# Optimization experiments

Hardware: AMD Instinct MI355X
Metric: run time of the kernel (lower is better)

Reference implementation:

```python
import jax, jax.numpy as jnp
import numpy as np

B = 32            # batch size
N = 100           # n_nodes (== MAX_N_NODES here)
MAXN = 100        # MAX_N_NODES
H = 256           # HIDDEN_DIM_FEATURES_EXTRACTOR
HA = 1024         # HIDDEN_DIM_ACTOR
HC = 512          # HIDDEN_DIM_CRITIC
K_ACTIVE = 5000   # exact number of active mask entries per batch element


def setup_inputs() -> dict:
    key = jax.random.key(0)
    ks = jax.random.split(key, 16)
    feat = jax.random.normal(ks[0], (B, N + 1, H), jnp.float32)
    # mask: exactly K_ACTIVE ones among N*N per batch row (dim == K for all rows)
    rng = np.random.default_rng(0)
    mask = np.zeros((B, N * N), np.float32)
    for i in range(B):
        mask[i, rng.choice(N * N, size=K_ACTIVE, replace=False)] = 1.0
    mask = jnp.asarray(mask).reshape(B, N, N)
    ext_mask = jnp.concatenate([jnp.zeros((B, 1, N), jnp.float32), mask], axis=1)  # [B, N+1, N]
    embedded_features = jnp.concatenate([feat, ext_mask], axis=2)  # [B, N+1, H+N]

    def lin(k, fi, fo):
        s = 1.0 / np.sqrt(fi)
        return (jax.random.uniform(k, (fi, fo), jnp.float32, -s, s),
                jax.random.uniform(jax.random.fold_in(k, 1), (fo,), jnp.float32, -s, s))

    aW1, ab1 = lin(ks[1], 3 * H, HA)
    aW2, ab2 = lin(ks[2], HA, HA)
    aW3, ab3 = lin(ks[3], HA, 1)
    cW1, cb1 = lin(ks[4], H, HC)
    cW2, cb2 = lin(ks[5], HC, HC)
    cW3, cb3 = lin(ks[6], HC, 1)
    return dict(embedded_features=embedded_features,
                aW1=aW1, ab1=ab1, aW2=aW2, ab2=ab2, aW3=aW3, ab3=ab3,
                cW1=cW1, cb1=cb1, cW2=cW2, cb2=cb2, cW3=cW3, cb3=cb3,
                K=K_ACTIVE)


def reference(embedded_features, aW1, ab1, aW2, ab2, aW3, ab3,
              cW1, cb1, cW2, cb2, cW3, cb3, K):
    # decompose features
    gn = embedded_features[:, :, :H]
    ext_mask = embedded_features[:, :, H:]
    g = gn[:, :1, :]                      # [B,1,H] graph embedding
    nodes = gn[:, 1:, :]                  # [B,N,H] node embeddings
    mask = ext_mask[:, 1:, :].reshape(B, -1)  # [B, N*N]

    # indexes of active pairs (stable top_k -> ascending indices among ones, like nonzero)
    _, idx = jax.lax.top_k(mask, K)       # [B,K] int32
    idx1 = idx // N
    idx2 = idx % N
    n1 = jnp.take_along_axis(nodes, idx1[:, :, None], axis=1)  # [B,K,H]
    n2 = jnp.take_along_axis(nodes, idx2[:, :, None], axis=1)  # [B,K,H]
    pairs = jnp.concatenate([jnp.broadcast_to(g, (B, K, H)), n1, n2], axis=-1)  # [B,K,3H]

    # actor MLP (tanh hidden activations)
    h = jnp.tanh(pairs @ aW1 + ab1)
    h = jnp.tanh(h @ aW2 + ab2)
    logits = h @ aW3 + ab3                # [B,K,1]
    pi = jax.nn.softmax(logits, axis=1)   # softmax over the K gathered pairs

    # scatter back into padded grid
    shaped = jnp.zeros((B, N * N), pi.dtype).at[jnp.arange(B)[:, None], idx].set(pi[..., 0])
    filled = jnp.zeros((B, MAXN, MAXN), pi.dtype).at[:, :N, :N].set(shaped.reshape(B, N, N))
    filled = filled.reshape(B, MAXN * MAXN)

    # critic MLP on graph embedding
    hv = jnp.tanh(g @ cW1 + cb1)
    hv = jnp.tanh(hv @ cW2 + cb2)
    value = hv @ cW3 + cb3                # [B,1,1]
    return filled, value
```

## Files before the change

### kernel.cpp

```cpp
#include <hip/hip_runtime.h>
#include <stdint.h>

#define AS1 __attribute__((address_space(1)))
#define AS3 __attribute__((address_space(3)))

typedef __bf16 bf16x8 __attribute__((ext_vector_type(8)));
typedef float  f32x4  __attribute__((ext_vector_type(4)));
typedef int    i32x4  __attribute__((ext_vector_type(4)));
typedef int    i32x8  __attribute__((ext_vector_type(8)));
typedef float  f32x16 __attribute__((ext_vector_type(16)));

__device__ __forceinline__ float tanh_fast(float x){
    float e = __expf(2.0f * x);
    return 1.0f - 2.0f * __builtin_amdgcn_rcpf(e + 1.0f);
}
__device__ __forceinline__ float tanh4_fast(float x){
    float e = __expf(2.0f * x);
    return fmaf(-8.0f, __builtin_amdgcn_rcpf(e + 1.0f), 4.0f);
}

__device__ __forceinline__ unsigned short f2bf(float f){
    unsigned int u = __float_as_uint(f);
    u = (u + 0x7fffu + ((u >> 16) & 1u)) >> 16;
    return (unsigned short)u;
}

template<int SEL>
__device__ __forceinline__ unsigned int pk4(unsigned int old, float a, float b){
#if defined(__has_builtin) && __has_builtin(__builtin_amdgcn_cvt_scalef32_pk_fp4_f32)
    return __builtin_amdgcn_cvt_scalef32_pk_fp4_f32(old, a, b, 1.0f, SEL);
#else
    float fa = fabsf(a), fb = fabsf(b);
    unsigned int ma = fa < 0.25f ? 0u : fa < 0.75f ? 1u : fa < 1.25f ? 2u :
                      fa < 1.75f ? 3u : fa < 2.5f  ? 4u : fa < 3.5f  ? 5u :
                      fa < 5.0f  ? 6u : 7u;
    unsigned int mb = fb < 0.25f ? 0u : fb < 0.75f ? 1u : fb < 1.25f ? 2u :
                      fb < 1.75f ? 3u : fb < 2.5f  ? 4u : fb < 3.5f  ? 5u :
                      fb < 5.0f  ? 6u : 7u;
    ma |= (a < 0.0f ? 8u : 0u); mb |= (b < 0.0f ? 8u : 0u);
    return old | ((ma | (mb << 4)) << (8 * SEL));
#endif
}

__device__ __forceinline__ i32x8 lo4(i32x4 a){
    return __builtin_shufflevector(a, a, 0, 1, 2, 3, -1, -1, -1, -1);
}

#define B2F(u, lo, hi) { lo = __uint_as_float((u) << 16); hi = __uint_as_float((u) & 0xffff0000u); }

__global__ __launch_bounds__(256) void k_stage1(
    const float* __restrict__ ef,  const float* __restrict__ aW1, const float* __restrict__ ab1,
    const float* __restrict__ aW2,
    const float* __restrict__ cW1, const float* __restrict__ cb1,
    const float* __restrict__ cW2, const float* __restrict__ cb2,
    const float* __restrict__ cW3, const float* __restrict__ cb3,
    int* __restrict__ pairs, unsigned char* __restrict__ w2b,
    unsigned short* __restrict__ P, float* __restrict__ out, int* __restrict__ qctr)
{
    int blk = blockIdx.x;
    int t = threadIdx.x;
    __shared__ __align__(16) unsigned short an[112 * 264];
    __shared__ float gsh[256], gpart[4][64];
    __shared__ int s_base, s_woff[4], s_wc[4];
    __shared__ float gs[256], h1[512], h2[512], wred[4];

    if (blk == 1024 && t == 0) qctr[0] = 0;

    if (blk < 1024){
        int cb = blk & 15, s = (blk >> 4) & 1, b = blk >> 5;
        for (int e = t; e < 25600; e += 256){
            int row = e >> 8, col = e & 255;
            an[row * 264 + col] = f2bf(ef[(size_t)b * 35956 + (size_t)(1 + row) * 356 + col]);
        }
        for (int e = t; e < 3168; e += 256) an[26400 + e] = 0;
        gsh[t] = ef[(size_t)b * 35956 + t];
        __syncthreads();

        if (s == 0){
            int cl = t & 63, q = t >> 6;
            const float* a1p = aW1 + (size_t)(q * 64) * 1024 + cb * 64 + cl;
            float p = 0.f;
            for (int i = 0; i < 64; ++i) p += gsh[q * 64 + i] * a1p[(size_t)i * 1024];
            gpart[q][cl] = p;
        }
        __syncthreads();

        int w = t >> 6, lane = t & 63, quad = lane >> 4, n = lane & 15;
        int c = cb * 64 + w * 16 + n;
        bf16x8 bfr[8];
        const float* wp = aW1 + (size_t)(256 + s * 256 + quad * 8) * 1024 + c;
#pragma unroll
        for (int kt = 0; kt < 8; ++kt){
            unsigned int ww[4];
#pragma unroll
            for (int jj = 0; jj < 4; ++jj){
                unsigned short lo = f2bf(wp[(size_t)(kt * 32 + 2 * jj) * 1024]);
                unsigned short hi = f2bf(wp[(size_t)(kt * 32 + 2 * jj + 1) * 1024]);
                ww[jj] = (unsigned int)lo | ((unsigned int)hi << 16);
            }
            uint4 pk = make_uint4(ww[0], ww[1], ww[2], ww[3]);
            bfr[kt] = *(bf16x8*)&pk;
        }
        f32x4 acc[7];
#pragma unroll
        for (int m = 0; m < 7; ++m){ f32x4 z = {0.f, 0.f, 0.f, 0.f}; acc[m] = z; }
#pragma unroll
        for (int kt = 0; kt < 8; ++kt){
#pragma unroll
            for (int m = 0; m < 7; ++m){
                const bf16x8* ap = (const bf16x8*)(an + (m * 16 + n) * 264 + kt * 32 + quad * 8);
                acc[m] = __builtin_amdgcn_mfma_f32_16x16x32_bf16(*ap, bfr[kt], acc[m], 0, 0, 0);
            }
        }
        int cw = w * 16 + n;
        float addv = (s == 0)
            ? (gpart[0][cw] + gpart[1][cw] + gpart[2][cw] + gpart[3][cw] + ab1[c]) : 0.0f;
        size_t base = (size_t)s * 3276800 + (size_t)b * 102400;
#pragma unroll
        for (int m = 0; m < 7; ++m){
            int r0 = m * 16 + quad * 4;
#pragma unroll
            for (int r = 0; r < 4; ++r){
                int row = r0 + r;
                if (row < 100) P[base + (size_t)row * 1024 + c] = f2bf(acc[m][r] + addv);
            }
        }
    } else if (blk < 1056){
        int b = blk - 1024;
        if (t == 0) s_base = 0;
        __syncthreads();
        int lane = t & 63, w = t >> 6;
        for (int ch = 0; ch < 40; ++ch){
            int pos = ch * 256 + t;
            bool valid = false;
            if (pos < 10000){
                int r = pos / 100, c = pos - (pos / 100) * 100;
                valid = ef[(size_t)b * 35956 + (size_t)(1 + r) * 356 + 256 + c] != 0.0f;
            }
            unsigned long long bal = __ballot(valid);
            if (lane == 0) s_wc[w] = __popcll(bal);
            __syncthreads();
            if (t == 0){
                int r = s_base;
                for (int q = 0; q < 4; ++q){ s_woff[q] = r; r += s_wc[q]; }
                s_base = r;
            }
            __syncthreads();
            if (valid){
                int rank = __popcll(bal & ((1ull << lane) - 1ull));
                int o = s_woff[w] + rank;
                if (o < 5000) pairs[b * 5000 + o] = pos;
            }
            __syncthreads();
        }
    } else if (blk < 1184){
        int tid = (blk - 1056) * 256 + t;
        int lane = tid & 63, kt = (tid >> 6) & 15, ct = tid >> 10;
        int lh = lane >> 5, n = lane & 31;
        const float* src = aW2 + (size_t)(kt * 64 + lh * 32) * 1024 + ct * 32 + n;
        unsigned int d[4] = {0u, 0u, 0u, 0u};
#pragma unroll
        for (int j = 0; j < 32; ++j){
            float a = src[(size_t)j * 1024] * 128.0f;
            float f = fabsf(a);
            unsigned int m = f < 0.25f ? 0u : f < 0.75f ? 1u : f < 1.25f ? 2u :
                             f < 1.75f ? 3u : f < 2.5f  ? 4u : f < 3.5f  ? 5u :
                             f < 5.0f  ? 6u : 7u;
            unsigned int nib = m | (a < 0.0f ? 8u : 0u);
            d[j >> 3] |= nib << (4 * (j & 7));
        }
        *(uint4*)(w2b + (size_t)(ct * 16 + kt) * 1024 + lane * 16) =
            make_uint4(d[0], d[1], d[2], d[3]);
    } else {
        int b = blk - 1184;
        gs[t] = ef[(size_t)b * 35956 + t];
        __syncthreads();
        for (int o = t; o < 512; o += 256){
            float a = cb1[o];
            for (int i = 0; i < 256; ++i) a += gs[i] * cW1[(size_t)i * 512 + o];
            h1[o] = tanh_fast(a);
        }
        __syncthreads();
        for (int o = t; o < 512; o += 256){
            float a = cb2[o];
            for (int i = 0; i < 512; ++i) a += h1[i] * cW2[(size_t)i * 512 + o];
            h2[o] = tanh_fast(a);
        }
        __syncthreads();
        float p = h2[t] * cW3[t] + h2[t + 256] * cW3[t + 256];
        for (int m = 32; m >= 1; m >>= 1) p += __shfl_xor(p, m);
        if ((t & 63) == 0) wred[t >> 6] = p;
        __syncthreads();
        if (t == 0) out[320000 + b] = wred[0] + wred[1] + wred[2] + wred[3] + cb3[0];
    }
}

__global__ __launch_bounds__(256, 4) void k_main(
    const int* __restrict__ pairs,
    const unsigned short* __restrict__ P1, const unsigned short* __restrict__ P2,
    const unsigned char* __restrict__ w2b, const float* __restrict__ ab2,
    const float* __restrict__ aW3, float* __restrict__ logits, int* __restrict__ qctr)
{
    __shared__ __align__(16) unsigned char wbuf[2][16384];
    __shared__ int s_tile;
    int t = threadIdx.x, w = t >> 6, lane = t & 63;
    int lrow = lane & 31, lh = lane >> 5;
    int soff = w * 4096 + lane * 16;

    for (;;){
        if (t == 0) s_tile = atomicAdd(qctr, 1);
        __syncthreads();
        int tt = s_tile;
        if (tt >= 1280) break;
        int b = tt / 40, tile = tt - b * 40;

        {
            const unsigned char* s = w2b + soff;
            unsigned char* d = &wbuf[0][0] + soff;
#pragma unroll
            for (int i = 0; i < 4; ++i)
                __builtin_amdgcn_global_load_lds((AS1 void*)(s + i * 1024),
                                                 (AS3 void*)(d + i * 1024), 16, 0, 0);
        }

        int grow = tile * 128 + w * 32 + lrow;
        int pidx = pairs[b * 5000 + (grow < 5000 ? grow : 4999)];
        int i1 = pidx / 100, i2 = pidx - i1 * 100;
        const uint4* pa = (const uint4*)(P1 + (((size_t)(b * 100 + i1)) << 10)) + lh * 4;
        const uint4* pb = (const uint4*)(P2 + (((size_t)(b * 100 + i2)) << 10)) + lh * 4;

        i32x4 af4[16];
#pragma unroll
        for (int kt = 0; kt < 16; ++kt){
            uint4 qa[4], qb[4];
#pragma unroll
            for (int j = 0; j < 4; ++j){ qa[j] = pa[kt * 8 + j]; qb[j] = pb[kt * 8 + j]; }
            unsigned int d[4];
#pragma unroll
            for (int j = 0; j < 4; ++j){
                float a0, a1, b0, b1;
                unsigned int dd = 0;
                B2F(qa[j].x, a0, a1); B2F(qb[j].x, b0, b1);
                dd = pk4<0>(dd, tanh4_fast(a0 + b0), tanh4_fast(a1 + b1));
                B2F(qa[j].y, a0, a1); B2F(qb[j].y, b0, b1);
                dd = pk4<1>(dd, tanh4_fast(a0 + b0), tanh4_fast(a1 + b1));
                B2F(qa[j].z, a0, a1); B2F(qb[j].z, b0, b1);
                dd = pk4<2>(dd, tanh4_fast(a0 + b0), tanh4_fast(a1 + b1));
                B2F(qa[j].w, a0, a1); B2F(qb[j].w, b0, b1);
                dd = pk4<3>(dd, tanh4_fast(a0 + b0), tanh4_fast(a1 + b1));
                d[j] = dd;
            }
            i32x4 f = {(int)d[0], (int)d[1], (int)d[2], (int)d[3]};
            af4[kt] = f;
        }

        float prt[16];
#pragma unroll
        for (int r = 0; r < 16; ++r) prt[r] = 0.f;
        f32x16 acc0, acc1;

        for (int ct = 0; ct < 32; ++ct){
            __syncthreads();
            if (ct < 31){
                const unsigned char* sp = w2b + (size_t)(ct + 1) * 16384 + soff;
                unsigned char* d = &wbuf[(ct + 1) & 1][0] + soff;
#pragma unroll
                for (int i = 0; i < 4; ++i)
                    __builtin_amdgcn_global_load_lds((AS1 void*)(sp + i * 1024),
                                                     (AS3 void*)(d + i * 1024), 16, 0, 0);
            }
#pragma unroll
            for (int r = 0; r < 16; ++r){ acc0[r] = 0.f; acc1[r] = 0.f; }
            const unsigned char* bb = &wbuf[ct & 1][0] + lane * 16;
#pragma unroll
            for (int j = 0; j < 8; ++j){
                uint4 q0 = *(const uint4*)(bb + (2 * j) * 1024);
                uint4 q1 = *(const uint4*)(bb + (2 * j + 1) * 1024);
                i32x4 b0 = {(int)q0.x, (int)q0.y, (int)q0.z, (int)q0.w};
                i32x4 b1 = {(int)q1.x, (int)q1.y, (int)q1.z, (int)q1.w};
                acc0 = __builtin_amdgcn_mfma_scale_f32_32x32x64_f8f6f4(
                           lo4(af4[2 * j]),     lo4(b0), acc0, 4, 4, 0, 0x7D7D7D7D, 0, 0x78787878);
                acc1 = __builtin_amdgcn_mfma_scale_f32_32x32x64_f8f6f4(
                           lo4(af4[2 * j + 1]), lo4(b1), acc1, 4, 4, 0, 0x7D7D7D7D, 0, 0x78787878);
            }
            int c = ct * 32 + lrow;
            float w3 = aW3[c], bias = ab2[c];
#pragma unroll
            for (int r = 0; r < 16; ++r)
                prt[r] += tanh_fast(acc0[r] + acc1[r] + bias) * w3;
        }

#pragma unroll
        for (int r = 0; r < 16; ++r){
            float v = prt[r];
            v += __shfl_xor(v, 1); v += __shfl_xor(v, 2); v += __shfl_xor(v, 4);
            v += __shfl_xor(v, 8); v += __shfl_xor(v, 16);
            if (lrow == 0){
                int row = (r & 3) + 8 * (r >> 2) + 4 * lh;
                int g = tile * 128 + w * 32 + row;
                if (g < 5000) logits[b * 5000 + g] = v;
            }
        }
    }
}

__global__ void k_soft(const float* __restrict__ logits, const int* __restrict__ pairs,
                       float* __restrict__ out){
    int b = blockIdx.x, t = threadIdx.x;
    __shared__ float red[4];
    __shared__ float bmS, bsS;
    float* ob = out + (size_t)b * 10000;
    for (int j = t; j < 10000; j += 256) ob[j] = 0.0f;
    const float* lg = logits + b * 5000;
    float m = -1e30f;
    for (int j = t; j < 5000; j += 256) m = fmaxf(m, lg[j]);
    for (int s = 32; s >= 1; s >>= 1) m = fmaxf(m, __shfl_xor(m, s));
    if ((t & 63) == 0) red[t >> 6] = m;
    __syncthreads();
    if (t == 0) bmS = fmaxf(fmaxf(red[0], red[1]), fmaxf(red[2], red[3]));
    __syncthreads();
    float mm = bmS;
    float s = 0.f;
    for (int j = t; j < 5000; j += 256) s += __expf(lg[j] - mm);
    for (int k = 32; k >= 1; k >>= 1) s += __shfl_xor(s, k);
    if ((t & 63) == 0) red[t >> 6] = s;
    __syncthreads();
    if (t == 0) bsS = 1.0f / (red[0] + red[1] + red[2] + red[3]);
    __syncthreads();
    float inv = bsS;
    for (int j = t; j < 5000; j += 256){
        int pos = pairs[b * 5000 + j];
        ob[pos] = __expf(lg[j] - mm) * inv;
    }
}

extern "C" void kernel_launch(void* const* d_in, const int* in_sizes, int n_in,
                              void* d_out, int out_size, void* d_ws, size_t ws_size,
                              hipStream_t stream) {
    (void)in_sizes; (void)n_in; (void)out_size; (void)ws_size;
    const float* ef  = (const float*)d_in[0];
    const float* aW1 = (const float*)d_in[1];
    const float* ab1 = (const float*)d_in[2];
    const float* aW2 = (const float*)d_in[3];
    const float* ab2 = (const float*)d_in[4];
    const float* aW3 = (const float*)d_in[5];
    const float* cW1 = (const float*)d_in[7];
    const float* cb1 = (const float*)d_in[8];
    const float* cW2 = (const float*)d_in[9];
    const float* cb2 = (const float*)d_in[10];
    const float* cW3 = (const float*)d_in[11];
    const float* cb3 = (const float*)d_in[12];
    float* out = (float*)d_out;
    char* ws = (char*)d_ws;
    int*   pairs  = (int*)(ws + 0);
    float* logits = (float*)(ws + 640000);
    unsigned short* P1 = (unsigned short*)(ws + 1411072);
    unsigned short* P2 = (unsigned short*)(ws + 7964672);
    unsigned char*  w2b = (unsigned char*)(ws + 14518272);
    int*   qctr   = (int*)(ws + 16615424);

    k_stage1<<<1216, 256, 0, stream>>>(ef, aW1, ab1, aW2, cW1, cb1, cW2, cb2, cW3, cb3,
                                       pairs, w2b, P1, out, qctr);
    k_main  <<<1024, 256, 0, stream>>>(pairs, P1, P2, w2b, ab2, aW3, logits, qctr);
    k_soft  <<<32,   256, 0, stream>>>(logits, pairs, out);
}
```

Baseline: 322.3 us.

## Merge stage1 halves per block and use single MFMA accumulator chain in main

Stage 1 now computes both node-projection halves (n1 and n2 weight slices) in one block. The shared-memory node tile is loaded once and each A fragment feeds two MFMAs, so the grid shrinks from 1216 to 704 blocks. This removes redundant node loading and bf16 conversion but doubles per-block register use and work. In the main kernel, the two interleaved accumulator chains become one serial chain of 16 MFMAs, which saves registers but lengthens the MFMA dependency chain.

```diff
diff --git a/kernel.cpp b/kernel.cpp
--- a/kernel.cpp
+++ b/kernel.cpp
@@ -64,10 +64,10 @@
     __shared__ int s_base, s_woff[4], s_wc[4];
     __shared__ float gs[256], h1[512], h2[512], wred[4];
 
-    if (blk == 1024 && t == 0) qctr[0] = 0;
-
-    if (blk < 1024){
-        int cb = blk & 15, s = (blk >> 4) & 1, b = blk >> 5;
+    if (blk == 512 && t == 0) qctr[0] = 0;
+
+    if (blk < 512){
+        int cb = blk & 15, b = blk >> 4;
         for (int e = t; e < 25600; e += 256){
             int row = e >> 8, col = e & 255;
             an[row * 264 + col] = f2bf(ef[(size_t)b * 35956 + (size_t)(1 + row) * 356 + col]);
@@ -76,7 +76,7 @@
         gsh[t] = ef[(size_t)b * 35956 + t];
         __syncthreads();
 
-        if (s == 0){
+        {
             int cl = t & 63, q = t >> 6;
             const float* a1p = aW1 + (size_t)(q * 64) * 1024 + cb * 64 + cl;
             float p = 0.f;
@@ -87,46 +87,54 @@
 
         int w = t >> 6, lane = t & 63, quad = lane >> 4, n = lane & 15;
         int c = cb * 64 + w * 16 + n;
-        bf16x8 bfr[8];
-        const float* wp = aW1 + (size_t)(256 + s * 256 + quad * 8) * 1024 + c;
+        bf16x8 bfr0[8], bfr1[8];
+        const float* wp0 = aW1 + (size_t)(256 + quad * 8) * 1024 + c;
+        const float* wp1 = aW1 + (size_t)(512 + quad * 8) * 1024 + c;
 #pragma unroll
         for (int kt = 0; kt < 8; ++kt){
-            unsigned int ww[4];
+            unsigned int w0[4], w1[4];
 #pragma unroll
             for (int jj = 0; jj < 4; ++jj){
-                unsigned short lo = f2bf(wp[(size_t)(kt * 32 + 2 * jj) * 1024]);
-                unsigned short hi = f2bf(wp[(size_t)(kt * 32 + 2 * jj + 1) * 1024]);
-                ww[jj] = (unsigned int)lo | ((unsigned int)hi << 16);
-            }
-            uint4 pk = make_uint4(ww[0], ww[1], ww[2], ww[3]);
-            bfr[kt] = *(bf16x8*)&pk;
-        }
-        f32x4 acc[7];
-#pragma unroll
-        for (int m = 0; m < 7; ++m){ f32x4 z = {0.f, 0.f, 0.f, 0.f}; acc[m] = z; }
+                size_t off0 = (size_t)(kt * 32 + 2 * jj) * 1024;
+                size_t off1 = off0 + 1024;
+                w0[jj] = (unsigned int)f2bf(wp0[off0]) | ((unsigned int)f2bf(wp0[off1]) << 16);
+                w1[jj] = (unsigned int)f2bf(wp1[off0]) | ((unsigned int)f2bf(wp1[off1]) << 16);
+            }
+            uint4 p0 = make_uint4(w0[0], w0[1], w0[2], w0[3]);
+            uint4 p1 = make_uint4(w1[0], w1[1], w1[2], w1[3]);
+            bfr0[kt] = *(bf16x8*)&p0;
+            bfr1[kt] = *(bf16x8*)&p1;
+        }
+        f32x4 acc0[7], acc1[7];
+#pragma unroll
+        for (int m = 0; m < 7; ++m){ f32x4 z = {0.f, 0.f, 0.f, 0.f}; acc0[m] = z; acc1[m] = z; }
 #pragma unroll
         for (int kt = 0; kt < 8; ++kt){
 #pragma unroll
             for (int m = 0; m < 7; ++m){
                 const bf16x8* ap = (const bf16x8*)(an + (m * 16 + n) * 264 + kt * 32 + quad * 8);
-                acc[m] = __builtin_amdgcn_mfma_f32_16x16x32_bf16(*ap, bfr[kt], acc[m], 0, 0, 0);
+                bf16x8 av = *ap;
+                acc0[m] = __builtin_amdgcn_mfma_f32_16x16x32_bf16(av, bfr0[kt], acc0[m], 0, 0, 0);
+                acc1[m] = __builtin_amdgcn_mfma_f32_16x16x32_bf16(av, bfr1[kt], acc1[m], 0, 0, 0);
             }
         }
         int cw = w * 16 + n;
-        float addv = (s == 0)
-            ? (gpart[0][cw] + gpart[1][cw] + gpart[2][cw] + gpart[3][cw] + ab1[c]) : 0.0f;
-        size_t base = (size_t)s * 3276800 + (size_t)b * 102400;
+        float addv = gpart[0][cw] + gpart[1][cw] + gpart[2][cw] + gpart[3][cw] + ab1[c];
+        size_t base = (size_t)b * 102400;
 #pragma unroll
         for (int m = 0; m < 7; ++m){
             int r0 = m * 16 + quad * 4;
 #pragma unroll
             for (int r = 0; r < 4; ++r){
                 int row = r0 + r;
-                if (row < 100) P[base + (size_t)row * 1024 + c] = f2bf(acc[m][r] + addv);
-            }
-        }
-    } else if (blk < 1056){
-        int b = blk - 1024;
+                if (row < 100){
+                    P[base + (size_t)row * 1024 + c]           = f2bf(acc0[m][r] + addv);
+                    P[3276800 + base + (size_t)row * 1024 + c] = f2bf(acc1[m][r]);
+                }
+            }
+        }
+    } else if (blk < 544){
+        int b = blk - 512;
         if (t == 0) s_base = 0;
         __syncthreads();
         int lane = t & 63, w = t >> 6;
@@ -153,8 +161,8 @@
             }
             __syncthreads();
         }
-    } else if (blk < 1184){
-        int tid = (blk - 1056) * 256 + t;
+    } else if (blk < 672){
+        int tid = (blk - 544) * 256 + t;
         int lane = tid & 63, kt = (tid >> 6) & 15, ct = tid >> 10;
         int lh = lane >> 5, n = lane & 31;
         const float* src = aW2 + (size_t)(kt * 64 + lh * 32) * 1024 + ct * 32 + n;
@@ -172,7 +180,7 @@
         *(uint4*)(w2b + (size_t)(ct * 16 + kt) * 1024 + lane * 16) =
             make_uint4(d[0], d[1], d[2], d[3]);
     } else {
-        int b = blk - 1184;
+        int b = blk - 672;
         gs[t] = ef[(size_t)b * 35956 + t];
         __syncthreads();
         for (int o = t; o < 512; o += 256){
@@ -257,7 +265,7 @@
         float prt[16];
 #pragma unroll
         for (int r = 0; r < 16; ++r) prt[r] = 0.f;
-        f32x16 acc0, acc1;
+        f32x16 acc;
 
         for (int ct = 0; ct < 32; ++ct){
             __syncthreads();
@@ -270,24 +278,20 @@
                                                      (AS3 void*)(d + i * 1024), 16, 0, 0);
             }
 #pragma unroll
-            for (int r = 0; r < 16; ++r){ acc0[r] = 0.f; acc1[r] = 0.f; }
+            for (int r = 0; r < 16; ++r) acc[r] = 0.f;
             const unsigned char* bb = &wbuf[ct & 1][0] + lane * 16;
 #pragma unroll
-            for (int j = 0; j < 8; ++j){
-                uint4 q0 = *(const uint4*)(bb + (2 * j) * 1024);
-                uint4 q1 = *(const uint4*)(bb + (2 * j + 1) * 1024);
-                i32x4 b0 = {(int)q0.x, (int)q0.y, (int)q0.z, (int)q0.w};
-                i32x4 b1 = {(int)q1.x, (int)q1.y, (int)q1.z, (int)q1.w};
-                acc0 = __builtin_amdgcn_mfma_scale_f32_32x32x64_f8f6f4(
-                           lo4(af4[2 * j]),     lo4(b0), acc0, 4, 4, 0, 0x7D7D7D7D, 0, 0x78787878);
-                acc1 = __builtin_amdgcn_mfma_scale_f32_32x32x64_f8f6f4(
-                           lo4(af4[2 * j + 1]), lo4(b1), acc1, 4, 4, 0, 0x7D7D7D7D, 0, 0x78787878);
+            for (int kt = 0; kt < 16; ++kt){
+                uint4 q = *(const uint4*)(bb + kt * 1024);
+                i32x4 bq = {(int)q.x, (int)q.y, (int)q.z, (int)q.w};
+                acc = __builtin_amdgcn_mfma_scale_f32_32x32x64_f8f6f4(
+                          lo4(af4[kt]), lo4(bq), acc, 4, 4, 0, 0x7D7D7D7D, 0, 0x78787878);
             }
             int c = ct * 32 + lrow;
             float w3 = aW3[c], bias = ab2[c];
 #pragma unroll
             for (int r = 0; r < 16; ++r)
-                prt[r] += tanh_fast(acc0[r] + acc1[r] + bias) * w3;
+                prt[r] += tanh_fast(acc[r] + bias) * w3;
         }
 
 #pragma unroll
@@ -359,7 +363,7 @@
     unsigned char*  w2b = (unsigned char*)(ws + 14518272);
     int*   qctr   = (int*)(ws + 16615424);
 
-    k_stage1<<<1216, 256, 0, stream>>>(ef, aW1, ab1, aW2, cW1, cb1, cW2, cb2, cW3, cb3,
+    k_stage1<<<704,  256, 0, stream>>>(ef, aW1, ab1, aW2, cW1, cb1, cW2, cb2, cW3, cb3,
                                        pairs, w2b, P1, out, qctr);
     k_main  <<<1024, 256, 0, stream>>>(pairs, P1, P2, w2b, ab2, aW3, logits, qctr);
     k_soft  <<<32,   256, 0, stream>>>(logits, pairs, out);
```

After: 307.7 us. 4.5% less time.
